# Kernel tuning notes

Measured on AMD Instinct MI355X. Metric: run time of the kernel, lower is better.

The kernel has to match this reference:

```python
import jax, jax.numpy as jnp
import numpy as np
from jax import lax

GAMMA = 0.1


def setup_inputs() -> dict:
    key = jax.random.key(0)
    k1, k2 = jax.random.split(key)
    pred = jax.random.normal(k1, (64, 512), dtype=jnp.float32)
    target = jax.random.normal(k2, (64, 512), dtype=jnp.float32)
    return {"pred": pred, "target": target}


def _soft_dtw(pred, target, gamma=GAMMA):
    # pred, target: [B, L]
    B, L = pred.shape
    inf = jnp.float32(jnp.inf)
    # pairwise squared distances: [B, L, L]
    dist = (pred[:, :, None] - target[:, None, :]) ** 2

    def softmin3(r0, r1, r2):
        # -gamma * logsumexp(-r/gamma) over the 3 predecessors (stable)
        s = jnp.stack([r0, r1, r2], axis=-1)
        return -gamma * jax.nn.logsumexp(-s / gamma, axis=-1)

    # R[0, :] = [0, inf, inf, ...]  (row 0 of the (L+1)x(L+1) DP table)
    init_row = jnp.concatenate(
        [jnp.zeros((B, 1), jnp.float32), jnp.full((B, L), inf, jnp.float32)], axis=1
    )  # [B, L+1]

    def row_step(prev_row, d_row):
        # prev_row: R[i-1, :] of shape [B, L+1]; d_row: dist[:, i-1, :] of shape [B, L]
        r0s = prev_row[:, :-1].T  # R[i-1, j-1], [L, B]
        r1s = prev_row[:, 1:].T   # R[i-1, j],   [L, B]
        ds = d_row.T              # [L, B]

        def cell(r_left, inp):
            r0, r1, d = inp
            val = d + softmin3(r0, r1, r_left)
            return val, val

        _, vals = lax.scan(cell, jnp.full((B,), inf, jnp.float32), (r0s, r1s, ds))
        new_row = jnp.concatenate([jnp.full((B, 1), inf, jnp.float32), vals.T], axis=1)
        return new_row, None

    # scan over rows i = 1..L; dist reordered to [L, B, L]
    last_row, _ = lax.scan(row_step, init_row, jnp.swapaxes(dist, 0, 1))
    return last_row[:, -1].mean()  # R[:, L, L].mean()


def reference(pred, target):
    return _soft_dtw(pred, target)
```

## Files before the change

kernel.cpp:

```cpp
#include <hip/hip_runtime.h>

#define LSEQ 512
#define NB 64
#define NCHUNK 51

__device__ __forceinline__ float dpp_shr1(float old, float x) {
  return __int_as_float(__builtin_amdgcn_update_dpp(
      __float_as_int(old), __float_as_int(x), 0x138, 0xF, 0xF, false));
}
__device__ __forceinline__ float dpp_shl1(float x) {
  return __int_as_float(__builtin_amdgcn_update_dpp(
      0, __float_as_int(x), 0x130, 0xF, 0xF, false));
}

__device__ __forceinline__ void renorm(float& d, float& e) {
  const int eb = __float_as_int(e);
  const int E = (eb >> 23) - 127;
  e = __int_as_float((eb & 0x007FFFFF) | 0x3F800000);
  d -= (float)E;
}

template <bool FULL>
__device__ __forceinline__ void chunk16(
    int cbase, const float* tg, const float2* ring2P, float2* ring2W, float p0,
    float p1, bool is_wr, int lane, float& v0d, float& v0e, float& v1d,
    float& v1e, float& r0d, float& r0e, float& tcur) {
  renorm(v0d, v0e);
  renorm(v1d, v1e);

  float tinj = tg[(cbase + (lane & 15)) & 511];
  const float2 rj = ring2P[(cbase + 1 + (lane & 15)) & 127];
  float rdinj = rj.x, reinj = rj.y;

  float vvd[16], vve[16];
#pragma unroll
  for (int u = 0; u < 16; ++u) {
    tcur = dpp_shr1(tinj, tcur);
    const float r1d = dpp_shr1(rdinj, v1d);
    const float r1e = dpp_shr1(reinj, v1e);
    if (u < 15) {
      tinj = dpp_shl1(tinj);
      rdinj = dpp_shl1(rdinj);
      reinj = dpp_shl1(reinj);
    }
    const float diff0 = p0 - tcur;
    const float M0 = fminf(fminf(r0d, r1d), v0d);
    const float d0 = __builtin_fmaf(diff0, diff0, M0);
    const float diff1 = p1 - tcur;
    const float M1 = fminf(fminf(v0d, d0), v1d);
    const float d1 = __builtin_fmaf(diff1, diff1, M1);
    const float a0 = M0 - r0d, a1 = M0 - r1d, a2 = M0 - v0d;
    const float b0 = M1 - v0d, b1 = M1 - d0, b2 = M1 - v1d;
    float x0, x1, x2, x3, x4, x5;
    asm volatile("v_exp_f32 %0, %1" : "=v"(x0) : "v"(a0));
    asm volatile("v_exp_f32 %0, %1" : "=v"(x1) : "v"(a1));
    asm volatile("v_exp_f32 %0, %1" : "=v"(x2) : "v"(a2));
    asm volatile("v_exp_f32 %0, %1" : "=v"(x3) : "v"(b0));
    asm volatile("v_exp_f32 %0, %1" : "=v"(x4) : "v"(b1));
    asm volatile("v_exp_f32 %0, %1" : "=v"(x5) : "v"(b2));
    const float e0 = __builtin_fmaf(
        x2, v0e, __builtin_fmaf(x1, r1e, x0 * r0e));
    const float e1 = __builtin_fmaf(
        x5, v1e, __builtin_fmaf(x4, e0, x3 * v0e));
    vvd[u] = d1;
    vve[u] = e1;
    if (FULL) {
      v0d = d0; v0e = e0; v1d = d1; v1e = e1;
    } else {
      const int j = cbase + 1 + u - lane;
      const bool act = ((unsigned)(j - 1)) < (unsigned)LSEQ;
      v0d = act ? d0 : v0d; v0e = act ? e0 : v0e;
      v1d = act ? d1 : v1d; v1e = act ? e1 : v1e;
    }
    r0d = r1d;
    r0e = r1e;
  }

  if (is_wr) {
    const int j0 = cbase - 62;
#pragma unroll
    for (int k = 0; k < 16; ++k) {
      if (FULL || (((unsigned)(j0 + k - 1)) < (unsigned)LSEQ))
        ring2W[(j0 + k) & 127] = make_float2(vvd[k], vve[k]);
    }
  }
}

__global__ __launch_bounds__(256) void dtw_band(
    const float* __restrict__ pred, const float* __restrict__ target,
    float* __restrict__ part) {
  const int b = blockIdx.x;
  const int tid = threadIdx.x;
  const int w = tid >> 6;
  const int lane = tid & 63;
  const bool is_wr = (lane == 63) && (w < 3);

  __shared__ float tg[LSEQ];
  __shared__ float2 rings2[4][128];

  const float SC = 3.79828146f;
  const float2 pp = ((const float2*)(pred + b * LSEQ))[tid];
  const float p0 = pp.x * SC, p1 = pp.y * SC;
  const float2 tt = ((const float2*)(target + b * LSEQ))[tid];
  ((float2*)tg)[tid] = make_float2(tt.x * SC, tt.y * SC);
  ((float2*)rings2)[tid] = make_float2(INFINITY, 1.0f);
  ((float2*)rings2)[tid + 256] = make_float2(INFINITY, 1.0f);

  const int lag = w * 80;
  const int cw0 = 5 * w;
  const float2* __restrict__ ring2P = rings2[w == 0 ? 3 : w - 1];
  float2* __restrict__ ring2W = rings2[w];

  float v0d = INFINITY, v0e = 1.0f;
  float v1d = INFINITY, v1e = 1.0f;
  float r0d = (tid == 0) ? 0.0f : INFINITY;
  float r0e = 1.0f;
  float tcur = 0.0f;

  for (int c = 0; c < NCHUNK; ++c) {
    __syncthreads();
    if (c < cw0 || c > cw0 + 35) continue;
    const int cbase = 16 * c - lag;
    if (c >= cw0 + 4 && c <= cw0 + 31)
      chunk16<true>(cbase, tg, ring2P, ring2W, p0, p1, is_wr, lane, v0d, v0e,
                    v1d, v1e, r0d, r0e, tcur);
    else
      chunk16<false>(cbase, tg, ring2P, ring2W, p0, p1, is_wr, lane, v0d, v0e,
                     v1d, v1e, r0d, r0e, tcur);
  }

  if (tid == 255)
    part[b] = (v1d - __builtin_amdgcn_logf(v1e)) * 0.069314718f;
}

__global__ void dtw_reduce(const float* __restrict__ part,
                           float* __restrict__ out) {
  float v = part[threadIdx.x];
#pragma unroll
  for (int o = 32; o > 0; o >>= 1) v += __shfl_down(v, o);
  if (threadIdx.x == 0) out[0] = v * (1.0f / NB);
}

extern "C" void kernel_launch(void* const* d_in, const int* in_sizes, int n_in,
                              void* d_out, int out_size, void* d_ws,
                              size_t ws_size, hipStream_t stream) {
  const float* pred = (const float*)d_in[0];
  const float* target = (const float*)d_in[1];
  float* part = (float*)d_ws;

  dtw_band<<<NB, 256, 0, stream>>>(pred, target, part);
  dtw_reduce<<<1, 64, 0, stream>>>(part, (float*)d_out);
}
```

Baseline: 90.48 us.

## Replace DPP injection shifts with per-lane LDS target loads and readlane broadcasts

Each lane now reads its 16 target values directly from a zero-padded shared array indexed by lane offset, instead of shifting them through the wavefront with DPP. The ring values from the previous wave are broadcast with readlane into scalar registers and fed as the injection operand of the single remaining DPP row-shift. This removes the three DPP shift-left ops per step and the tcur carry from the serial dependency chain. The cost is 16 LDS loads per chunk and 32 readlanes, plus extra registers. The inline-asm v_exp_f32 calls are also replaced with the exp2 builtin, which lets the compiler schedule them.

```diff
diff --git a/kernel.cpp b/kernel.cpp
--- a/kernel.cpp
+++ b/kernel.cpp
@@ -4,13 +4,13 @@
 #define NB 64
 #define NCHUNK 51
 
-__device__ __forceinline__ float dpp_shr1(float old, float x) {
+__device__ __forceinline__ float dpp_shr1_inj(float inj, float x) {
   return __int_as_float(__builtin_amdgcn_update_dpp(
-      __float_as_int(old), __float_as_int(x), 0x138, 0xF, 0xF, false));
+      __float_as_int(inj), __float_as_int(x), 0x138, 0xF, 0xF, false));
 }
-__device__ __forceinline__ float dpp_shl1(float x) {
-  return __int_as_float(__builtin_amdgcn_update_dpp(
-      0, __float_as_int(x), 0x130, 0xF, 0xF, false));
+
+__device__ __forceinline__ float rdlane(float x, int u) {
+  return __int_as_float(__builtin_amdgcn_readlane(__float_as_int(x), u));
 }
 
 __device__ __forceinline__ void renorm(float& d, float& e) {
@@ -22,46 +22,45 @@
 
 template <bool FULL>
 __device__ __forceinline__ void chunk16(
-    int cbase, const float* tg, const float2* ring2P, float2* ring2W, float p0,
-    float p1, bool is_wr, int lane, float& v0d, float& v0e, float& v1d,
-    float& v1e, float& r0d, float& r0e, float& tcur) {
+    int cbase, const float* tgpad, const float2* ring2P, float2* ring2W,
+    float p0, float p1, bool is_wr, int lane, float& v0d, float& v0e,
+    float& v1d, float& v1e, float& r0d, float& r0e) {
   renorm(v0d, v0e);
   renorm(v1d, v1e);
 
-  float tinj = tg[(cbase + (lane & 15)) & 511];
+  float tt[16];
+  const int tb = 64 + cbase - lane;
+#pragma unroll
+  for (int k = 0; k < 16; ++k) tt[k] = tgpad[tb + k];
+
   const float2 rj = ring2P[(cbase + 1 + (lane & 15)) & 127];
-  float rdinj = rj.x, reinj = rj.y;
+  float sjd[16], sje[16];
+#pragma unroll
+  for (int k = 0; k < 16; ++k) {
+    sjd[k] = rdlane(rj.x, k);
+    sje[k] = rdlane(rj.y, k);
+  }
 
   float vvd[16], vve[16];
 #pragma unroll
   for (int u = 0; u < 16; ++u) {
-    tcur = dpp_shr1(tinj, tcur);
-    const float r1d = dpp_shr1(rdinj, v1d);
-    const float r1e = dpp_shr1(reinj, v1e);
-    if (u < 15) {
-      tinj = dpp_shl1(tinj);
-      rdinj = dpp_shl1(rdinj);
-      reinj = dpp_shl1(reinj);
-    }
-    const float diff0 = p0 - tcur;
+    const float r1d = dpp_shr1_inj(sjd[u], v1d);
+    const float r1e = dpp_shr1_inj(sje[u], v1e);
+    const float tcu = tt[u];
+    const float diff0 = p0 - tcu;
     const float M0 = fminf(fminf(r0d, r1d), v0d);
     const float d0 = __builtin_fmaf(diff0, diff0, M0);
-    const float diff1 = p1 - tcur;
+    const float diff1 = p1 - tcu;
     const float M1 = fminf(fminf(v0d, d0), v1d);
     const float d1 = __builtin_fmaf(diff1, diff1, M1);
-    const float a0 = M0 - r0d, a1 = M0 - r1d, a2 = M0 - v0d;
-    const float b0 = M1 - v0d, b1 = M1 - d0, b2 = M1 - v1d;
-    float x0, x1, x2, x3, x4, x5;
-    asm volatile("v_exp_f32 %0, %1" : "=v"(x0) : "v"(a0));
-    asm volatile("v_exp_f32 %0, %1" : "=v"(x1) : "v"(a1));
-    asm volatile("v_exp_f32 %0, %1" : "=v"(x2) : "v"(a2));
-    asm volatile("v_exp_f32 %0, %1" : "=v"(x3) : "v"(b0));
-    asm volatile("v_exp_f32 %0, %1" : "=v"(x4) : "v"(b1));
-    asm volatile("v_exp_f32 %0, %1" : "=v"(x5) : "v"(b2));
-    const float e0 = __builtin_fmaf(
-        x2, v0e, __builtin_fmaf(x1, r1e, x0 * r0e));
-    const float e1 = __builtin_fmaf(
-        x5, v1e, __builtin_fmaf(x4, e0, x3 * v0e));
+    const float x0 = __builtin_amdgcn_exp2f(M0 - r0d);
+    const float x1 = __builtin_amdgcn_exp2f(M0 - r1d);
+    const float x2 = __builtin_amdgcn_exp2f(M0 - v0d);
+    const float x3 = __builtin_amdgcn_exp2f(M1 - v0d);
+    const float x4 = __builtin_amdgcn_exp2f(M1 - d0);
+    const float x5 = __builtin_amdgcn_exp2f(M1 - v1d);
+    const float e0 = __builtin_fmaf(x2, v0e, __builtin_fmaf(x1, r1e, x0 * r0e));
+    const float e1 = __builtin_fmaf(x5, v1e, __builtin_fmaf(x4, e0, x3 * v0e));
     vvd[u] = d1;
     vve[u] = e1;
     if (FULL) {
@@ -95,14 +94,18 @@
   const int lane = tid & 63;
   const bool is_wr = (lane == 63) && (w < 3);
 
-  __shared__ float tg[LSEQ];
+  __shared__ float tgpad[640];
   __shared__ float2 rings2[4][128];
 
   const float SC = 3.79828146f;
   const float2 pp = ((const float2*)(pred + b * LSEQ))[tid];
   const float p0 = pp.x * SC, p1 = pp.y * SC;
   const float2 tt = ((const float2*)(target + b * LSEQ))[tid];
-  ((float2*)tg)[tid] = make_float2(tt.x * SC, tt.y * SC);
+  ((float2*)(tgpad + 64))[tid] = make_float2(tt.x * SC, tt.y * SC);
+  if (tid < 64) {
+    tgpad[tid] = 0.0f;
+    tgpad[576 + tid] = 0.0f;
+  }
   ((float2*)rings2)[tid] = make_float2(INFINITY, 1.0f);
   ((float2*)rings2)[tid + 256] = make_float2(INFINITY, 1.0f);
 
@@ -115,18 +118,17 @@
   float v1d = INFINITY, v1e = 1.0f;
   float r0d = (tid == 0) ? 0.0f : INFINITY;
   float r0e = 1.0f;
-  float tcur = 0.0f;
 
   for (int c = 0; c < NCHUNK; ++c) {
     __syncthreads();
     if (c < cw0 || c > cw0 + 35) continue;
     const int cbase = 16 * c - lag;
     if (c >= cw0 + 4 && c <= cw0 + 31)
-      chunk16<true>(cbase, tg, ring2P, ring2W, p0, p1, is_wr, lane, v0d, v0e,
-                    v1d, v1e, r0d, r0e, tcur);
+      chunk16<true>(cbase, tgpad, ring2P, ring2W, p0, p1, is_wr, lane, v0d,
+                    v0e, v1d, v1e, r0d, r0e);
     else
-      chunk16<false>(cbase, tg, ring2P, ring2W, p0, p1, is_wr, lane, v0d, v0e,
-                     v1d, v1e, r0d, r0e, tcur);
+      chunk16<false>(cbase, tgpad, ring2P, ring2W, p0, p1, is_wr, lane, v0d,
+                     v0e, v1d, v1e, r0d, r0e);
   }
 
   if (tid == 255)
```

Result: no change. 89.36 us (-1.2%).
